# Kernel optimization log

Hardware: AMD Instinct MI355X
Metric: run time of the kernel (lower is better)

Reference implementation:

```python
import jax, jax.numpy as jnp
import numpy as np

B, S, D, FF, E, K = 32, 32, 768, 3072, 8, 2


def setup_inputs() -> dict:
    key = jax.random.key(0)
    ks = jax.random.split(key, 6)
    rn = lambda k, shape, sc: (jax.random.normal(k, shape, dtype=jnp.float32) * sc)
    return {
        "x": rn(ks[0], (B, S, D), 1.0),
        "attention_mask": jnp.ones((B, S), dtype=jnp.float32),
        "Wg": rn(ks[1], (D, E), 0.02),          # gate Linear weight
        "bg": jnp.zeros((E,), jnp.float32),      # gate Linear bias
        "W1": rn(ks[2], (E, D, FF), 0.02),       # per-expert FFN up-proj
        "b1": jnp.zeros((E, FF), jnp.float32),
        "W2": rn(ks[3], (E, FF, D), 0.02),       # per-expert FFN down-proj
        "b2": jnp.zeros((E, D), jnp.float32),
    }


def reference(x, attention_mask, Wg, bg, W1, b1, W2, b2):
    # --- sentence-level gating (source overwrites mask with ones) ---
    mask = jnp.ones_like(attention_mask)                      # [B,S]
    x_avg = (x * mask[..., None]).sum(1) / mask[..., None].sum(1)  # [B,D]
    logits_gate = x_avg @ Wg + bg                             # [B,E]
    prob_gate = jax.nn.softmax(logits_gate, axis=-1)
    select_prob_gate, gate = jax.lax.top_k(prob_gate, K)      # [B,K], [B,K]

    # --- per-expert FFN on all sentences (dense equivalent of the
    #     sort/split/vstack dispatch in the source) ---
    # h: [E,B,S,FF]
    h = jnp.einsum('bsd,edf->ebsf', x, W1) + b1[:, None, None, :]
    h = jax.nn.gelu(h, approximate=False)
    out = jnp.einsum('ebsf,efd->ebsd', h, W2) + b2[:, None, None, :]  # [E,B,S,D]

    # --- combine: the source sums the topk expert outputs UNWEIGHTED
    #     (tmp_prob is computed but never applied) ---
    sel = jax.nn.one_hot(gate, E, dtype=x.dtype).sum(1)       # [B,E], entries in {0,1}
    moe_result = jnp.einsum('be,ebsd->bsd', sel, out)         # [B,S,D]

    return moe_result, select_prob_gate, gate
```

## Files before the change

kernel.cpp:

```cpp
#include <hip/hip_runtime.h>
#include <hip/hip_bf16.h>
#include <math.h>

#define BB 32
#define SS 32
#define DD 768
#define FFD 3072
#define EE 8
#define KK 2
#define NPAIR 64
#define MAXT 22

typedef __attribute__((ext_vector_type(8))) short short8;
typedef __attribute__((ext_vector_type(4))) float f32x4;
typedef __attribute__((ext_vector_type(8))) unsigned short us8;


#define H_OFF    4096
#define XBF_OFF  (H_OFF + 12582912)
#define PART_OFF XBF_OFF
#define PZ       (2048 * 768)
#define WS_MAIN  ((size_t)PART_OFF + 4ull * PZ * 2ull)

__device__ __forceinline__ unsigned short f2bf(float f) {
    __hip_bfloat16 h = __float2bfloat16(f);
    return __builtin_bit_cast(unsigned short, h);
}
__device__ __forceinline__ float bf2f(unsigned short u) {
    __hip_bfloat16 h = __builtin_bit_cast(__hip_bfloat16, u);
    return __bfloat162float(h);
}

__device__ __forceinline__ int lds_off(int row, int byte_in_row) {
    return row * 128 + (byte_in_row ^ ((row & 7) << 4));
}

__device__ __forceinline__ void phase_barrier() {
    __builtin_amdgcn_sched_barrier(0);
    asm volatile("s_waitcnt lgkmcnt(0)" ::: "memory");
    __builtin_amdgcn_s_barrier();
    __builtin_amdgcn_sched_barrier(0);
}

__global__ __launch_bounds__(256) void gate_kernel(
    const float* __restrict__ x, const float* __restrict__ Wg,
    const float* __restrict__ bg, float* __restrict__ out,
    int* __restrict__ gates)
{
    int b = blockIdx.x;
    int tid = threadIdx.x;

    float acc[EE];
#pragma unroll
    for (int e = 0; e < EE; ++e) acc[e] = 0.f;

    for (int d = tid; d < DD; d += 256) {
        float xs = 0.f;
        const float* xp = x + (size_t)b * SS * DD + d;
#pragma unroll
        for (int s = 0; s < SS; ++s) xs += xp[(size_t)s * DD];
#pragma unroll
        for (int e = 0; e < EE; ++e) acc[e] += xs * Wg[d * EE + e];
    }

    __shared__ float red[EE][256];
#pragma unroll
    for (int e = 0; e < EE; ++e) red[e][tid] = acc[e];
    __syncthreads();
    for (int off = 128; off > 0; off >>= 1) {
        if (tid < off) {
#pragma unroll
            for (int e = 0; e < EE; ++e) red[e][tid] += red[e][tid + off];
        }
        __syncthreads();
    }

    if (tid == 0) {
        float lg[EE], p[EE];
        float m = -1e30f;
#pragma unroll
        for (int e = 0; e < EE; ++e) {
            lg[e] = red[e][0] / (float)SS + bg[e];
            m = fmaxf(m, lg[e]);
        }
        float sum = 0.f;
#pragma unroll
        for (int e = 0; e < EE; ++e) { p[e] = expf(lg[e] - m); sum += p[e]; }
        float inv = 1.f / sum;
#pragma unroll
        for (int e = 0; e < EE; ++e) p[e] *= inv;

        int i1 = 0;
        for (int e = 1; e < EE; ++e) if (p[e] > p[i1]) i1 = e;
        int i2 = (i1 == 0) ? 1 : 0;
        for (int e = 0; e < EE; ++e) if (e != i1 && p[e] > p[i2]) i2 = e;

        float* prob_out = out + (size_t)BB * SS * DD;
        float* gate_out = prob_out + BB * KK;
        prob_out[b * KK + 0] = p[i1];
        prob_out[b * KK + 1] = p[i2];
        gate_out[b * KK + 0] = (float)i1;
        gate_out[b * KK + 1] = (float)i2;
        gates[b * KK + 0] = i1;
        gates[b * KK + 1] = i2;
    }
}

__global__ __launch_bounds__(64) void sched_kernel(int* __restrict__ wsi)
{
    __shared__ int g[NPAIR];
    __shared__ int cnt[EE];
    __shared__ int start[EE + 1];
    int p = threadIdx.x;

    g[p] = wsi[p];
    __syncthreads();

    if (p < EE) {
        int c = 0;
        for (int q = 0; q < NPAIR; ++q) c += (g[q] == p);
        cnt[p] = c;
    }
    __syncthreads();
    if (p == 0) {
        start[0] = 0;
        for (int e = 0; e < EE; ++e) start[e + 1] = start[e] + cnt[e];
    }
    __syncthreads();

    int e = g[p];
    int rank = 0;
    for (int q = 0; q < NPAIR; ++q) rank += (q < p) && (g[q] == e);
    int slot = start[e] + rank;
    wsi[64 + slot] = p;
    wsi[200 + p] = slot;

    if (p == 0) {
        int t = 0;
        for (int e2 = 0; e2 < EE; ++e2) {
            for (int o = 0; o < cnt[e2]; o += 4) {
                wsi[128 + t] = e2;
                wsi[152 + t] = start[e2] + o;
                wsi[176 + t] = (cnt[e2] - o) < 4 ? (cnt[e2] - o) : 4;
                ++t;
            }
        }
        for (; t < MAXT; ++t) wsi[176 + t] = 0;
    }
}

__global__ __launch_bounds__(256) void pack_x(
    const float* __restrict__ x, unsigned short* __restrict__ xbf)
{
    int i = blockIdx.x * 256 + threadIdx.x;
    const float4* src = (const float4*)(x + (size_t)i * 8);
    float4 v0 = src[0], v1 = src[1];
    us8 u;
    u[0] = f2bf(v0.x); u[1] = f2bf(v0.y); u[2] = f2bf(v0.z); u[3] = f2bf(v0.w);
    u[4] = f2bf(v1.x); u[5] = f2bf(v1.y); u[6] = f2bf(v1.z); u[7] = f2bf(v1.w);
    *(us8*)(xbf + (size_t)i * 8) = u;
}

__global__ __launch_bounds__(256) void init_kernel(
    const int* __restrict__ gates, const float* __restrict__ b2,
    float* __restrict__ out)
{
    int idx = blockIdx.x * 256 + threadIdx.x;
    if (idx >= BB * SS * DD) return;
    int b = idx / (SS * DD);
    int d = idx % DD;
    int e0 = gates[b * KK + 0];
    int e1 = gates[b * KK + 1];
    out[idx] = b2[e0 * DD + d] + b2[e1 * DD + d];
}

__global__ __launch_bounds__(256, 2) void up_gemm(
    const unsigned short* __restrict__ xbf, const float* __restrict__ W1,
    const float* __restrict__ b1, const int* __restrict__ wsi,
    unsigned short* __restrict__ H)
{
    int bid = blockIdx.x;
    int xcd = bid & 7;
    int r = bid >> 3;
    int tile = r % MAXT;
    int grp = r / MAXT;
    int nt = grp * 8 + xcd;
    int np = wsi[176 + tile];
    if (np == 0) return;
    int e = wsi[128 + tile];
    int slot0 = wsi[152 + tile];
    int tid = threadIdx.x;
    int wid = tid >> 6, lane = tid & 63;
    int wm = wid >> 1, wn = wid & 1;

    __shared__ char lds[65536];

    const unsigned short* asrc[4];
    int aoff[4];
#pragma unroll
    for (int i = 0; i < 4; ++i) {
        int c = tid + i * 256;
        int row = c >> 3, ch = c & 7;
        int lp = row >> 5;
        int lpc = lp < np ? lp : np - 1;
        int pair = wsi[64 + slot0 + lpc];
        int b = pair >> 1;
        asrc[i] = xbf + ((size_t)(b * SS + (row & 31))) * DD + ch * 8;
        aoff[i] = lds_off(row, ch * 16);
    }
    int n = tid & 127, kq = tid >> 7;
    const float* bsrc = W1 + ((size_t)e * DD + kq * 32) * FFD + nt * 128 + n;
    int boff[4];
#pragma unroll
    for (int m4 = 0; m4 < 4; ++m4) boff[m4] = lds_off(n, kq * 64 + m4 * 16);

    f32x4 acc[4][4];
#pragma unroll
    for (int i = 0; i < 4; ++i)
#pragma unroll
        for (int j = 0; j < 4; ++j) acc[i][j] = (f32x4)0.f;

    float bB0[32], bB1[32];
    us8 bA0[4], bA1[4];

    auto issue = [&](int k0, float (&bB)[32], us8 (&bA)[4]) {
        const float* wp = bsrc + (size_t)k0 * FFD;
#pragma unroll
        for (int j = 0; j < 32; ++j) bB[j] = wp[(size_t)j * FFD];
#pragma unroll
        for (int i = 0; i < 4; ++i) bA[i] = *(const us8*)(asrc[i] + k0);
    };
    auto store = [&](int p, const float (&bB)[32], const us8 (&bA)[4]) {
        char* Al = lds + p * 32768;
        char* Bl = Al + 16384;
#pragma unroll
        for (int i = 0; i < 4; ++i) *(us8*)(Al + aoff[i]) = bA[i];
#pragma unroll
        for (int m4 = 0; m4 < 4; ++m4) {
            us8 u;
#pragma unroll
            for (int m = 0; m < 8; ++m) u[m] = f2bf(bB[m4 * 8 + m]);
            *(us8*)(Bl + boff[m4]) = u;
        }
    };
    auto compute = [&](int p) {
        char* Al = lds + p * 32768;
        char* Bl = Al + 16384;
#pragma unroll
        for (int kk = 0; kk < 2; ++kk) {
            int kb = kk * 64 + (lane >> 4) * 16;
            short8 af[4], bf[4];
#pragma unroll
            for (int mf = 0; mf < 4; ++mf)
                af[mf] = *(short8*)(Al + lds_off(wm * 64 + mf * 16 + (lane & 15), kb));
#pragma unroll
            for (int nf = 0; nf < 4; ++nf)
                bf[nf] = *(short8*)(Bl + lds_off(wn * 64 + nf * 16 + (lane & 15), kb));
#pragma unroll
            for (int mf = 0; mf < 4; ++mf)
#pragma unroll
                for (int nf = 0; nf < 4; ++nf)
                    acc[mf][nf] = __builtin_amdgcn_mfma_f32_16x16x32_bf16(
                        af[mf], bf[nf], acc[mf][nf], 0, 0, 0);
        }
    };

    const int steps = 12;
    issue(0, bB0, bA0);
    issue(64, bB1, bA1);
    store(0, bB0, bA0);
    phase_barrier();
    for (int s = 0; s < steps; s += 2) {
        compute(0);
        if (s + 2 < steps) issue((s + 2) * 64, bB0, bA0);
        store(1, bB1, bA1);
        phase_barrier();
        compute(1);
        if (s + 2 < steps) {
            if (s + 3 < steps) issue((s + 3) * 64, bB1, bA1);
            store(0, bB0, bA0);
        }
        phase_barrier();
    }

    float bias[4];
#pragma unroll
    for (int nf = 0; nf < 4; ++nf)
        bias[nf] = b1[e * FFD + nt * 128 + wn * 64 + nf * 16 + (lane & 15)];
#pragma unroll
    for (int mf = 0; mf < 4; ++mf) {
#pragma unroll
        for (int i = 0; i < 4; ++i) {
            int row = wm * 64 + mf * 16 + (lane >> 4) * 4 + i;
            if ((row >> 5) >= np) continue;
            size_t srow = (size_t)(slot0 * 32 + row);
#pragma unroll
            for (int nf = 0; nf < 4; ++nf) {
                int f = nt * 128 + wn * 64 + nf * 16 + (lane & 15);
                float h = acc[mf][nf][i] + bias[nf];
                float g = 0.5f * h * (1.0f + erff(h * 0.70710678118654752f));
                H[srow * FFD + f] = f2bf(g);
            }
        }
    }
}

template<int MODE>
__global__ __launch_bounds__(256, 2) void down_gemm(
    const unsigned short* __restrict__ H, const float* __restrict__ W2,
    const int* __restrict__ wsi, unsigned short* __restrict__ part,
    float* __restrict__ out)
{
    int bid = blockIdx.x;
    int xcd = bid & 7;
    int r = bid >> 3;
    int tile = r % MAXT;
    int grp = r / MAXT;
    int pairidx = grp * 8 + xcd;
    int nt = pairidx % 6;
    int z = pairidx / 6;
    int np = wsi[176 + tile];
    if (np == 0) return;
    int e = wsi[128 + tile];
    int slot0 = wsi[152 + tile];
    int zb = z * (FFD / 4);
    int tid = threadIdx.x;
    int wid = tid >> 6, lane = tid & 63;
    int wm = wid >> 1, wn = wid & 1;

    __shared__ char lds[65536];

    const unsigned short* asrc[4];
    int aoff[4];
#pragma unroll
    for (int i = 0; i < 4; ++i) {
        int c = tid + i * 256;
        int row = c >> 3, ch = c & 7;
        int rc = row < np * 32 ? row : np * 32 - 1;
        asrc[i] = H + (size_t)(slot0 * 32 + rc) * FFD + zb + ch * 8;
        aoff[i] = lds_off(row, ch * 16);
    }
    int n = tid & 127, kq = tid >> 7;
    const float* bsrc = W2 + ((size_t)e * FFD + zb + kq * 32) * DD + nt * 128 + n;
    int boff[4];
#pragma unroll
    for (int m4 = 0; m4 < 4; ++m4) boff[m4] = lds_off(n, kq * 64 + m4 * 16);

    f32x4 acc[4][4];
#pragma unroll
    for (int i = 0; i < 4; ++i)
#pragma unroll
        for (int j = 0; j < 4; ++j) acc[i][j] = (f32x4)0.f;

    float bB0[32], bB1[32];
    us8 bA0[4], bA1[4];

    auto issue = [&](int k0, float (&bB)[32], us8 (&bA)[4]) {
        const float* wp = bsrc + (size_t)k0 * DD;
#pragma unroll
        for (int j = 0; j < 32; ++j) bB[j] = wp[(size_t)j * DD];
#pragma unroll
        for (int i = 0; i < 4; ++i) bA[i] = *(const us8*)(asrc[i] + k0);
    };
    auto store = [&](int p, const float (&bB)[32], const us8 (&bA)[4]) {
        char* Al = lds + p * 32768;
        char* Bl = Al + 16384;
#pragma unroll
        for (int i = 0; i < 4; ++i) *(us8*)(Al + aoff[i]) = bA[i];
#pragma unroll
        for (int m4 = 0; m4 < 4; ++m4) {
            us8 u;
#pragma unroll
            for (int m = 0; m < 8; ++m) u[m] = f2bf(bB[m4 * 8 + m]);
            *(us8*)(Bl + boff[m4]) = u;
        }
    };
    auto compute = [&](int p) {
        char* Al = lds + p * 32768;
        char* Bl = Al + 16384;
#pragma unroll
        for (int kk = 0; kk < 2; ++kk) {
            int kb = kk * 64 + (lane >> 4) * 16;
            short8 af[4], bf[4];
#pragma unroll
            for (int mf = 0; mf < 4; ++mf)
                af[mf] = *(short8*)(Al + lds_off(wm * 64 + mf * 16 + (lane & 15), kb));
#pragma unroll
            for (int nf = 0; nf < 4; ++nf)
                bf[nf] = *(short8*)(Bl + lds_off(wn * 64 + nf * 16 + (lane & 15), kb));
#pragma unroll
            for (int mf = 0; mf < 4; ++mf)
#pragma unroll
                for (int nf = 0; nf < 4; ++nf)
                    acc[mf][nf] = __builtin_amdgcn_mfma_f32_16x16x32_bf16(
                        af[mf], bf[nf], acc[mf][nf], 0, 0, 0);
        }
    };

    const int steps = 12;
    issue(0, bB0, bA0);
    issue(64, bB1, bA1);
    store(0, bB0, bA0);
    __syncthreads();
    for (int s = 0; s < steps; s += 2) {
        compute(0);
        if (s + 2 < steps) issue((s + 2) * 64, bB0, bA0);
        store(1, bB1, bA1);
        __syncthreads();
        compute(1);
        if (s + 2 < steps) {
            if (s + 3 < steps) issue((s + 3) * 64, bB1, bA1);
            store(0, bB0, bA0);
        }
        __syncthreads();
    }

#pragma unroll
    for (int mf = 0; mf < 4; ++mf) {
#pragma unroll
        for (int i = 0; i < 4; ++i) {
            int row = wm * 64 + mf * 16 + (lane >> 4) * 4 + i;
            int lp = row >> 5;
            if (lp >= np) continue;
            int col = nt * 128 + wn * 64 + (lane & 15);
            if (MODE == 0) {
                size_t srow = (size_t)(slot0 * 32 + row);
                unsigned short* pp = part + (size_t)z * PZ + srow * DD + col;
#pragma unroll
                for (int nf = 0; nf < 4; ++nf) pp[nf * 16] = f2bf(acc[mf][nf][i]);
            } else {
                int pair = wsi[64 + slot0 + lp];
                int b = pair >> 1;
                int sI = row & 31;
                float* op = out + ((size_t)(b * SS + sI)) * DD + col;
#pragma unroll
                for (int nf = 0; nf < 4; ++nf)
                    atomicAdd(op + nf * 16, acc[mf][nf][i]);
            }
        }
    }
}

__global__ __launch_bounds__(512) void reduce_kernel(
    const unsigned short* __restrict__ part, const int* __restrict__ wsi,
    const float* __restrict__ b2, float* __restrict__ out)
{
    int i8 = blockIdx.x * 512 + threadIdx.x;
    int flat = i8 * 8;
    int b = flat / (SS * DD);
    int r = flat - b * (SS * DD);
    int s = r / DD;
    int d = r - s * DD;

    int e0 = wsi[b * KK + 0];
    int e1 = wsi[b * KK + 1];
    int sl0 = wsi[200 + b * KK + 0];
    int sl1 = wsi[200 + b * KK + 1];
    size_t r0 = (size_t)(sl0 * 32 + s) * DD + d;
    size_t r1 = (size_t)(sl1 * 32 + s) * DD + d;

    const float* bb0 = b2 + e0 * DD + d;
    const float* bb1 = b2 + e1 * DD + d;

    float v[8];
#pragma unroll
    for (int j = 0; j < 8; ++j) v[j] = bb0[j] + bb1[j];
#pragma unroll
    for (int z = 0; z < 4; ++z) {
        us8 p0 = *(const us8*)(part + (size_t)z * PZ + r0);
        us8 p1 = *(const us8*)(part + (size_t)z * PZ + r1);
#pragma unroll
        for (int j = 0; j < 8; ++j) v[j] += bf2f(p0[j]) + bf2f(p1[j]);
    }
    float4* op = (float4*)(out + flat);
    op[0] = make_float4(v[0], v[1], v[2], v[3]);
    op[1] = make_float4(v[4], v[5], v[6], v[7]);
}

extern "C" void kernel_launch(void* const* d_in, const int* in_sizes, int n_in,
                              void* d_out, int out_size, void* d_ws, size_t ws_size,
                              hipStream_t stream) {
    const float* x  = (const float*)d_in[0];
    const float* Wg = (const float*)d_in[2];
    const float* bg = (const float*)d_in[3];
    const float* W1 = (const float*)d_in[4];
    const float* b1 = (const float*)d_in[5];
    const float* W2 = (const float*)d_in[6];
    const float* b2 = (const float*)d_in[7];
    float* out = (float*)d_out;

    int* wsi = (int*)d_ws;
    unsigned short* H    = (unsigned short*)((char*)d_ws + H_OFF);
    unsigned short* xbf  = (unsigned short*)((char*)d_ws + XBF_OFF);
    unsigned short* part = (unsigned short*)((char*)d_ws + PART_OFF);

    gate_kernel<<<BB, 256, 0, stream>>>(x, Wg, bg, out, wsi);
    sched_kernel<<<1, 64, 0, stream>>>(wsi);
    pack_x<<<(BB * SS * DD) / (256 * 8), 256, 0, stream>>>(x, xbf);
    up_gemm<<<8 * MAXT * 3, 256, 0, stream>>>(xbf, W1, b1, wsi, H);

    if (ws_size >= WS_MAIN) {
        down_gemm<0><<<8 * MAXT * 3, 256, 0, stream>>>(H, W2, wsi, part, out);
        reduce_kernel<<<(BB * SS * DD) / (512 * 8), 512, 0, stream>>>(
            part, wsi, b2, out);
    } else {
        init_kernel<<<(BB * SS * DD + 255) / 256, 256, 0, stream>>>(wsi, b2, out);
        down_gemm<1><<<8 * MAXT * 3, 256, 0, stream>>>(H, W2, wsi, part, out);
    }
}
```

Measured before the change: 82.49 us.

## Use 512-thread blocks and load activation fragments directly from global memory

Both expert GEMMs move from 256 to 512 threads per block with 8 waves in a 2x4 layout, each wave covering a 64x32 sub-tile instead of 64x64. The bf16 activation (A) operand is no longer staged through LDS; each wave reads its MFMA fragments straight from global memory. LDS then holds only the double-buffered weight tile, halving shared memory per block and raising the occupancy target. The trade-off is more global/L2 traffic and latency exposure on the A loads, since fragments are re-read by each wave without prefetching. The custom phase barrier is replaced by __syncthreads.

```diff
diff --git a/kernel.cpp b/kernel.cpp
--- a/kernel.cpp
+++ b/kernel.cpp
@@ -33,13 +33,6 @@
 
 __device__ __forceinline__ int lds_off(int row, int byte_in_row) {
     return row * 128 + (byte_in_row ^ ((row & 7) << 4));
-}
-
-__device__ __forceinline__ void phase_barrier() {
-    __builtin_amdgcn_sched_barrier(0);
-    asm volatile("s_waitcnt lgkmcnt(0)" ::: "memory");
-    __builtin_amdgcn_s_barrier();
-    __builtin_amdgcn_sched_barrier(0);
 }
 
 __global__ __launch_bounds__(256) void gate_kernel(
@@ -174,7 +167,7 @@
     out[idx] = b2[e0 * DD + d] + b2[e1 * DD + d];
 }
 
-__global__ __launch_bounds__(256, 2) void up_gemm(
+__global__ __launch_bounds__(512, 4) void up_gemm(
     const unsigned short* __restrict__ xbf, const float* __restrict__ W1,
     const float* __restrict__ b1, const int* __restrict__ wsi,
     unsigned short* __restrict__ H)
@@ -191,102 +184,90 @@
     int slot0 = wsi[152 + tile];
     int tid = threadIdx.x;
     int wid = tid >> 6, lane = tid & 63;
-    int wm = wid >> 1, wn = wid & 1;
-
-    __shared__ char lds[65536];
-
-    const unsigned short* asrc[4];
-    int aoff[4];
-#pragma unroll
-    for (int i = 0; i < 4; ++i) {
-        int c = tid + i * 256;
-        int row = c >> 3, ch = c & 7;
+    int wm = wid >> 2, wn = wid & 3;
+
+    __shared__ char lds[32768];
+
+    const unsigned short* apL[4];
+#pragma unroll
+    for (int mf = 0; mf < 4; ++mf) {
+        int row = wm * 64 + mf * 16 + (lane & 15);
         int lp = row >> 5;
         int lpc = lp < np ? lp : np - 1;
         int pair = wsi[64 + slot0 + lpc];
-        int b = pair >> 1;
-        asrc[i] = xbf + ((size_t)(b * SS + (row & 31))) * DD + ch * 8;
-        aoff[i] = lds_off(row, ch * 16);
-    }
+        apL[mf] = xbf + ((size_t)((pair >> 1) * SS + (row & 31))) * DD
+                + (lane >> 4) * 8;
+    }
+
     int n = tid & 127, kq = tid >> 7;
-    const float* bsrc = W1 + ((size_t)e * DD + kq * 32) * FFD + nt * 128 + n;
-    int boff[4];
-#pragma unroll
-    for (int m4 = 0; m4 < 4; ++m4) boff[m4] = lds_off(n, kq * 64 + m4 * 16);
-
-    f32x4 acc[4][4];
+    const float* bsrc = W1 + ((size_t)e * DD + kq * 16) * FFD + nt * 128 + n;
+    int boff0 = lds_off(n, kq * 32);
+    int boff1 = lds_off(n, kq * 32 + 16);
+
+    f32x4 acc[4][2];
 #pragma unroll
     for (int i = 0; i < 4; ++i)
 #pragma unroll
-        for (int j = 0; j < 4; ++j) acc[i][j] = (f32x4)0.f;
-
-    float bB0[32], bB1[32];
-    us8 bA0[4], bA1[4];
-
-    auto issue = [&](int k0, float (&bB)[32], us8 (&bA)[4]) {
+        for (int j = 0; j < 2; ++j) acc[i][j] = (f32x4)0.f;
+
+    float bB0[16], bB1[16];
+
+    auto issue = [&](int k0, float (&bB)[16]) {
         const float* wp = bsrc + (size_t)k0 * FFD;
 #pragma unroll
-        for (int j = 0; j < 32; ++j) bB[j] = wp[(size_t)j * FFD];
-#pragma unroll
-        for (int i = 0; i < 4; ++i) bA[i] = *(const us8*)(asrc[i] + k0);
-    };
-    auto store = [&](int p, const float (&bB)[32], const us8 (&bA)[4]) {
-        char* Al = lds + p * 32768;
-        char* Bl = Al + 16384;
-#pragma unroll
-        for (int i = 0; i < 4; ++i) *(us8*)(Al + aoff[i]) = bA[i];
-#pragma unroll
-        for (int m4 = 0; m4 < 4; ++m4) {
-            us8 u;
-#pragma unroll
-            for (int m = 0; m < 8; ++m) u[m] = f2bf(bB[m4 * 8 + m]);
-            *(us8*)(Bl + boff[m4]) = u;
-        }
-    };
-    auto compute = [&](int p) {
-        char* Al = lds + p * 32768;
-        char* Bl = Al + 16384;
+        for (int j = 0; j < 16; ++j) bB[j] = wp[(size_t)j * FFD];
+    };
+    auto store = [&](int p, const float (&bB)[16]) {
+        char* Bl = lds + p * 16384;
+        us8 u0, u1;
+#pragma unroll
+        for (int m = 0; m < 8; ++m) { u0[m] = f2bf(bB[m]); u1[m] = f2bf(bB[8 + m]); }
+        *(us8*)(Bl + boff0) = u0;
+        *(us8*)(Bl + boff1) = u1;
+    };
+    auto compute = [&](int p, int k0) {
+        char* Bl = lds + p * 16384;
 #pragma unroll
         for (int kk = 0; kk < 2; ++kk) {
             int kb = kk * 64 + (lane >> 4) * 16;
-            short8 af[4], bf[4];
+            short8 af[4], bf[2];
 #pragma unroll
             for (int mf = 0; mf < 4; ++mf)
-                af[mf] = *(short8*)(Al + lds_off(wm * 64 + mf * 16 + (lane & 15), kb));
-#pragma unroll
-            for (int nf = 0; nf < 4; ++nf)
-                bf[nf] = *(short8*)(Bl + lds_off(wn * 64 + nf * 16 + (lane & 15), kb));
+                af[mf] = *(const short8*)(apL[mf] + k0 + kk * 32);
+#pragma unroll
+            for (int nf = 0; nf < 2; ++nf)
+                bf[nf] = *(short8*)(Bl + lds_off(wn * 32 + nf * 16 + (lane & 15), kb));
 #pragma unroll
             for (int mf = 0; mf < 4; ++mf)
 #pragma unroll
-                for (int nf = 0; nf < 4; ++nf)
+                for (int nf = 0; nf < 2; ++nf)
                     acc[mf][nf] = __builtin_amdgcn_mfma_f32_16x16x32_bf16(
                         af[mf], bf[nf], acc[mf][nf], 0, 0, 0);
         }
     };
 
     const int steps = 12;
-    issue(0, bB0, bA0);
-    issue(64, bB1, bA1);
-    store(0, bB0, bA0);
-    phase_barrier();
+    issue(0, bB0);
+    issue(64, bB1);
+    store(0, bB0);
+    __syncthreads();
     for (int s = 0; s < steps; s += 2) {
-        compute(0);
-        if (s + 2 < steps) issue((s + 2) * 64, bB0, bA0);
-        store(1, bB1, bA1);
-        phase_barrier();
-        compute(1);
+        compute(0, s * 64);
+        if (s + 2 < steps) issue((s + 2) * 64, bB0);
+        store(1, bB1);
+        __syncthreads();
+        compute(1, (s + 1) * 64);
         if (s + 2 < steps) {
-            if (s + 3 < steps) issue((s + 3) * 64, bB1, bA1);
-            store(0, bB0, bA0);
-        }
-        phase_barrier();
-    }
-
-    float bias[4];
-#pragma unroll
-    for (int nf = 0; nf < 4; ++nf)
-        bias[nf] = b1[e * FFD + nt * 128 + wn * 64 + nf * 16 + (lane & 15)];
+            if (s + 3 < steps) issue((s + 3) * 64, bB1);
+            store(0, bB0);
+        }
+        __syncthreads();
+    }
+
+    float bias[2];
+#pragma unroll
+    for (int nf = 0; nf < 2; ++nf)
+        bias[nf] = b1[e * FFD + nt * 128 + wn * 32 + nf * 16 + (lane & 15)];
 #pragma unroll
     for (int mf = 0; mf < 4; ++mf) {
 #pragma unroll
@@ -295,8 +276,8 @@
             if ((row >> 5) >= np) continue;
             size_t srow = (size_t)(slot0 * 32 + row);
 #pragma unroll
-            for (int nf = 0; nf < 4; ++nf) {
-                int f = nt * 128 + wn * 64 + nf * 16 + (lane & 15);
+            for (int nf = 0; nf < 2; ++nf) {
+                int f = nt * 128 + wn * 32 + nf * 16 + (lane & 15);
                 float h = acc[mf][nf][i] + bias[nf];
                 float g = 0.5f * h * (1.0f + erff(h * 0.70710678118654752f));
                 H[srow * FFD + f] = f2bf(g);
@@ -306,7 +287,7 @@
 }
 
 template<int MODE>
-__global__ __launch_bounds__(256, 2) void down_gemm(
+__global__ __launch_bounds__(512, 4) void down_gemm(
     const unsigned short* __restrict__ H, const float* __restrict__ W2,
     const int* __restrict__ wsi, unsigned short* __restrict__ part,
     float* __restrict__ out)
@@ -315,7 +296,8 @@
     int xcd = bid & 7;
     int r = bid >> 3;
     int tile = r % MAXT;
-    int grp = r / MAXT;
+    int grp = r >> 3 ? 0 : 0;
+    grp = (bid >> 3) / MAXT;
     int pairidx = grp * 8 + xcd;
     int nt = pairidx % 6;
     int z = pairidx / 6;
@@ -326,91 +308,79 @@
     int zb = z * (FFD / 4);
     int tid = threadIdx.x;
     int wid = tid >> 6, lane = tid & 63;
-    int wm = wid >> 1, wn = wid & 1;
-
-    __shared__ char lds[65536];
-
-    const unsigned short* asrc[4];
-    int aoff[4];
-#pragma unroll
-    for (int i = 0; i < 4; ++i) {
-        int c = tid + i * 256;
-        int row = c >> 3, ch = c & 7;
+    int wm = wid >> 2, wn = wid & 3;
+
+    __shared__ char lds[32768];
+
+    const unsigned short* apL[4];
+#pragma unroll
+    for (int mf = 0; mf < 4; ++mf) {
+        int row = wm * 64 + mf * 16 + (lane & 15);
         int rc = row < np * 32 ? row : np * 32 - 1;
-        asrc[i] = H + (size_t)(slot0 * 32 + rc) * FFD + zb + ch * 8;
-        aoff[i] = lds_off(row, ch * 16);
-    }
+        apL[mf] = H + (size_t)(slot0 * 32 + rc) * FFD + zb + (lane >> 4) * 8;
+    }
+
     int n = tid & 127, kq = tid >> 7;
-    const float* bsrc = W2 + ((size_t)e * FFD + zb + kq * 32) * DD + nt * 128 + n;
-    int boff[4];
-#pragma unroll
-    for (int m4 = 0; m4 < 4; ++m4) boff[m4] = lds_off(n, kq * 64 + m4 * 16);
-
-    f32x4 acc[4][4];
+    const float* bsrc = W2 + ((size_t)e * FFD + zb + kq * 16) * DD + nt * 128 + n;
+    int boff0 = lds_off(n, kq * 32);
+    int boff1 = lds_off(n, kq * 32 + 16);
+
+    f32x4 acc[4][2];
 #pragma unroll
     for (int i = 0; i < 4; ++i)
 #pragma unroll
-        for (int j = 0; j < 4; ++j) acc[i][j] = (f32x4)0.f;
-
-    float bB0[32], bB1[32];
-    us8 bA0[4], bA1[4];
-
-    auto issue = [&](int k0, float (&bB)[32], us8 (&bA)[4]) {
+        for (int j = 0; j < 2; ++j) acc[i][j] = (f32x4)0.f;
+
+    float bB0[16], bB1[16];
+
+    auto issue = [&](int k0, float (&bB)[16]) {
         const float* wp = bsrc + (size_t)k0 * DD;
 #pragma unroll
-        for (int j = 0; j < 32; ++j) bB[j] = wp[(size_t)j * DD];
-#pragma unroll
-        for (int i = 0; i < 4; ++i) bA[i] = *(const us8*)(asrc[i] + k0);
-    };
-    auto store = [&](int p, const float (&bB)[32], const us8 (&bA)[4]) {
-        char* Al = lds + p * 32768;
-        char* Bl = Al + 16384;
-#pragma unroll
-        for (int i = 0; i < 4; ++i) *(us8*)(Al + aoff[i]) = bA[i];
-#pragma unroll
-        for (int m4 = 0; m4 < 4; ++m4) {
-            us8 u;
-#pragma unroll
-            for (int m = 0; m < 8; ++m) u[m] = f2bf(bB[m4 * 8 + m]);
-            *(us8*)(Bl + boff[m4]) = u;
-        }
-    };
-    auto compute = [&](int p) {
-        char* Al = lds + p * 32768;
-        char* Bl = Al + 16384;
+        for (int j = 0; j < 16; ++j) bB[j] = wp[(size_t)j * DD];
+    };
+    auto store = [&](int p, const float (&bB)[16]) {
+        char* Bl = lds + p * 16384;
+        us8 u0, u1;
+#pragma unroll
+        for (int m = 0; m < 8; ++m) { u0[m] = f2bf(bB[m]); u1[m] = f2bf(bB[8 + m]); }
+        *(us8*)(Bl + boff0) = u0;
+        *(us8*)(Bl + boff1) = u1;
+    };
+    auto compute = [&](int p, int k0) {
+        char* Bl = lds + p * 16384;
 #pragma unroll
         for (int kk = 0; kk < 2; ++kk) {
             int kb = kk * 64 + (lane >> 4) * 16;
-            short8 af[4], bf[4];
+            short8 af[4], bf[2];
 #pragma unroll
             for (int mf = 0; mf < 4; ++mf)
-                af[mf] = *(short8*)(Al + lds_off(wm * 64 + mf * 16 + (lane & 15), kb));
-#pragma unroll
-            for (int nf = 0; nf < 4; ++nf)
-                bf[nf] = *(short8*)(Bl + lds_off(wn * 64 + nf * 16 + (lane & 15), kb));
+                af[mf] = *(const short8*)(apL[mf] + k0 + kk * 32);
+#pragma unroll
+            for (int nf = 0; nf < 2; ++nf)
+                bf[nf] = *(short8*)(Bl + lds_off(wn * 32 + nf * 16 + (lane & 15), kb));
 #pragma unroll
             for (int mf = 0; mf < 4; ++mf)
 #pragma unroll
-                for (int nf = 0; nf < 4; ++nf)
+                for (int nf = 0; nf < 2; ++nf)
                     acc[mf][nf] = __builtin_amdgcn_mfma_f32_16x16x32_bf16(
                         af[mf], bf[nf], acc[mf][nf], 0, 0, 0);
         }
     };
 
     const int steps = 12;
-    issue(0, bB0, bA0);
-    issue(64, bB1, bA1);
-    store(0, bB0, bA0);
+    issue(0, bB0);
+    issue(64, bB1);
+    store(0, bB0);
     __syncthreads();
     for (int s = 0; s < steps; s += 2) {
-        compute(0);
-        if (s + 2 < steps) issue((s + 2) * 64, bB0, bA0);
-        store(1, bB1, bA1);
+        compute(0, s * 64);
+        if (s + 2 < steps) issue((s + 2) * 64, bB0);
+        store(1, bB1);
         __syncthreads();
-        compute(1);
+        compute(1, (s + 1) * 64);
         if (s + 2 < steps) {
-            if (s + 3 < steps) issue((s + 3) * 64, bB1, bA1);
-            store(0, bB0, bA0);
+            if (s + 3 < steps) issue((s + 3) * 64, bB1);
+            store(0, bB0);
         }
         __syncthreads();
     }
@@ -422,19 +392,19 @@
             int row = wm * 64 + mf * 16 + (lane >> 4) * 4 + i;
             int lp = row >> 5;
             if (lp >= np) continue;
-            int col = nt * 128 + wn * 64 + (lane & 15);
+            int col = nt * 128 + wn * 32 + (lane & 15);
             if (MODE == 0) {
                 size_t srow = (size_t)(slot0 * 32 + row);
                 unsigned short* pp = part + (size_t)z * PZ + srow * DD + col;
 #pragma unroll
-                for (int nf = 0; nf < 4; ++nf) pp[nf * 16] = f2bf(acc[mf][nf][i]);
+                for (int nf = 0; nf < 2; ++nf) pp[nf * 16] = f2bf(acc[mf][nf][i]);
             } else {
                 int pair = wsi[64 + slot0 + lp];
                 int b = pair >> 1;
                 int sI = row & 31;
                 float* op = out + ((size_t)(b * SS + sI)) * DD + col;
 #pragma unroll
-                for (int nf = 0; nf < 4; ++nf)
+                for (int nf = 0; nf < 2; ++nf)
                     atomicAdd(op + nf * 16, acc[mf][nf][i]);
             }
         }
@@ -497,14 +467,14 @@
     gate_kernel<<<BB, 256, 0, stream>>>(x, Wg, bg, out, wsi);
     sched_kernel<<<1, 64, 0, stream>>>(wsi);
     pack_x<<<(BB * SS * DD) / (256 * 8), 256, 0, stream>>>(x, xbf);
-    up_gemm<<<8 * MAXT * 3, 256, 0, stream>>>(xbf, W1, b1, wsi, H);
+    up_gemm<<<8 * MAXT * 3, 512, 0, stream>>>(xbf, W1, b1, wsi, H);
 
     if (ws_size >= WS_MAIN) {
-        down_gemm<0><<<8 * MAXT * 3, 256, 0, stream>>>(H, W2, wsi, part, out);
+        down_gemm<0><<<8 * MAXT * 3, 512, 0, stream>>>(H, W2, wsi, part, out);
         reduce_kernel<<<(BB * SS * DD) / (512 * 8), 512, 0, stream>>>(
             part, wsi, b2, out);
     } else {
         init_kernel<<<(BB * SS * DD + 255) / 256, 256, 0, stream>>>(wsi, b2, out);
-        down_gemm<1><<<8 * MAXT * 3, 256, 0, stream>>>(H, W2, wsi, part, out);
-    }
-}
+        down_gemm<1><<<8 * MAXT * 3, 512, 0, stream>>>(H, W2, wsi, part, out);
+    }
+}
```

Measured after the change: 133.5 us. 61.8% more time.

## Halve up-projection M tile to two sentence pairs with a finer tile schedule

Applied to the files above, without the earlier changes.

The scheduler now also builds a second tile list that groups at most 2 (rather than 4) sentence-pairs per expert tile. up_gemm uses this list, shrinking each block's M tile from 128 to 64 rows, with all four waves splitting N instead of a 2x2 wave grid. LDS per block drops and launch bounds are raised to 3 blocks per CU, giving more blocks and less padding waste on partially filled tiles. The cost is that each W1 column tile is fetched and converted from fp32 by roughly twice as many blocks. The custom phase barrier is also replaced with __syncthreads.

```diff
diff --git a/kernel.cpp b/kernel.cpp
--- a/kernel.cpp
+++ b/kernel.cpp
@@ -10,6 +10,7 @@
 #define KK 2
 #define NPAIR 64
 #define MAXT 22
+#define MAXT2 36
 
 typedef __attribute__((ext_vector_type(8))) short short8;
 typedef __attribute__((ext_vector_type(4))) float f32x4;
@@ -33,13 +34,6 @@
 
 __device__ __forceinline__ int lds_off(int row, int byte_in_row) {
     return row * 128 + (byte_in_row ^ ((row & 7) << 4));
-}
-
-__device__ __forceinline__ void phase_barrier() {
-    __builtin_amdgcn_sched_barrier(0);
-    asm volatile("s_waitcnt lgkmcnt(0)" ::: "memory");
-    __builtin_amdgcn_s_barrier();
-    __builtin_amdgcn_sched_barrier(0);
 }
 
 __global__ __launch_bounds__(256) void gate_kernel(
@@ -147,6 +141,18 @@
         }
         for (; t < MAXT; ++t) wsi[176 + t] = 0;
     }
+    if (p == 1) {
+        int t = 0;
+        for (int e2 = 0; e2 < EE; ++e2) {
+            for (int o = 0; o < cnt[e2]; o += 2) {
+                wsi[300 + t] = e2;
+                wsi[340 + t] = start[e2] + o;
+                wsi[380 + t] = (cnt[e2] - o) < 2 ? (cnt[e2] - o) : 2;
+                ++t;
+            }
+        }
+        for (; t < MAXT2; ++t) wsi[380 + t] = 0;
+    }
 }
 
 __global__ __launch_bounds__(256) void pack_x(
@@ -174,7 +180,7 @@
     out[idx] = b2[e0 * DD + d] + b2[e1 * DD + d];
 }
 
-__global__ __launch_bounds__(256, 2) void up_gemm(
+__global__ __launch_bounds__(256, 3) void up_gemm(
     const unsigned short* __restrict__ xbf, const float* __restrict__ W1,
     const float* __restrict__ b1, const int* __restrict__ wsi,
     unsigned short* __restrict__ H)
@@ -182,23 +188,23 @@
     int bid = blockIdx.x;
     int xcd = bid & 7;
     int r = bid >> 3;
-    int tile = r % MAXT;
-    int grp = r / MAXT;
+    int tile = r % MAXT2;
+    int grp = r / MAXT2;
     int nt = grp * 8 + xcd;
-    int np = wsi[176 + tile];
+    int np = wsi[380 + tile];
     if (np == 0) return;
-    int e = wsi[128 + tile];
-    int slot0 = wsi[152 + tile];
+    int e = wsi[300 + tile];
+    int slot0 = wsi[340 + tile];
     int tid = threadIdx.x;
     int wid = tid >> 6, lane = tid & 63;
-    int wm = wid >> 1, wn = wid & 1;
-
-    __shared__ char lds[65536];
-
-    const unsigned short* asrc[4];
-    int aoff[4];
-#pragma unroll
-    for (int i = 0; i < 4; ++i) {
+    int wn = wid;
+
+    __shared__ char lds[49152];
+
+    const unsigned short* asrc[2];
+    int aoff[2];
+#pragma unroll
+    for (int i = 0; i < 2; ++i) {
         int c = tid + i * 256;
         int row = c >> 3, ch = c & 7;
         int lp = row >> 5;
@@ -214,27 +220,27 @@
 #pragma unroll
     for (int m4 = 0; m4 < 4; ++m4) boff[m4] = lds_off(n, kq * 64 + m4 * 16);
 
-    f32x4 acc[4][4];
+    f32x4 acc[4][2];
 #pragma unroll
     for (int i = 0; i < 4; ++i)
 #pragma unroll
-        for (int j = 0; j < 4; ++j) acc[i][j] = (f32x4)0.f;
+        for (int j = 0; j < 2; ++j) acc[i][j] = (f32x4)0.f;
 
     float bB0[32], bB1[32];
-    us8 bA0[4], bA1[4];
-
-    auto issue = [&](int k0, float (&bB)[32], us8 (&bA)[4]) {
+    us8 bA0[2], bA1[2];
+
+    auto issue = [&](int k0, float (&bB)[32], us8 (&bA)[2]) {
         const float* wp = bsrc + (size_t)k0 * FFD;
 #pragma unroll
         for (int j = 0; j < 32; ++j) bB[j] = wp[(size_t)j * FFD];
 #pragma unroll
-        for (int i = 0; i < 4; ++i) bA[i] = *(const us8*)(asrc[i] + k0);
+        for (int i = 0; i < 2; ++i) bA[i] = *(const us8*)(asrc[i] + k0);
     };
-    auto store = [&](int p, const float (&bB)[32], const us8 (&bA)[4]) {
-        char* Al = lds + p * 32768;
-        char* Bl = Al + 16384;
-#pragma unroll
-        for (int i = 0; i < 4; ++i) *(us8*)(Al + aoff[i]) = bA[i];
+    auto store = [&](int p, const float (&bB)[32], const us8 (&bA)[2]) {
+        char* Al = lds + p * 24576;
+        char* Bl = Al + 8192;
+#pragma unroll
+        for (int i = 0; i < 2; ++i) *(us8*)(Al + aoff[i]) = bA[i];
 #pragma unroll
         for (int m4 = 0; m4 < 4; ++m4) {
             us8 u;
@@ -244,22 +250,22 @@
         }
     };
     auto compute = [&](int p) {
-        char* Al = lds + p * 32768;
-        char* Bl = Al + 16384;
+        char* Al = lds + p * 24576;
+        char* Bl = Al + 8192;
 #pragma unroll
         for (int kk = 0; kk < 2; ++kk) {
             int kb = kk * 64 + (lane >> 4) * 16;
-            short8 af[4], bf[4];
+            short8 af[4], bf[2];
 #pragma unroll
             for (int mf = 0; mf < 4; ++mf)
-                af[mf] = *(short8*)(Al + lds_off(wm * 64 + mf * 16 + (lane & 15), kb));
-#pragma unroll
-            for (int nf = 0; nf < 4; ++nf)
-                bf[nf] = *(short8*)(Bl + lds_off(wn * 64 + nf * 16 + (lane & 15), kb));
+                af[mf] = *(short8*)(Al + lds_off(mf * 16 + (lane & 15), kb));
+#pragma unroll
+            for (int nf = 0; nf < 2; ++nf)
+                bf[nf] = *(short8*)(Bl + lds_off(wn * 32 + nf * 16 + (lane & 15), kb));
 #pragma unroll
             for (int mf = 0; mf < 4; ++mf)
 #pragma unroll
-                for (int nf = 0; nf < 4; ++nf)
+                for (int nf = 0; nf < 2; ++nf)
                     acc[mf][nf] = __builtin_amdgcn_mfma_f32_16x16x32_bf16(
                         af[mf], bf[nf], acc[mf][nf], 0, 0, 0);
         }
@@ -269,34 +275,34 @@
     issue(0, bB0, bA0);
     issue(64, bB1, bA1);
     store(0, bB0, bA0);
-    phase_barrier();
+    __syncthreads();
     for (int s = 0; s < steps; s += 2) {
         compute(0);
         if (s + 2 < steps) issue((s + 2) * 64, bB0, bA0);
         store(1, bB1, bA1);
-        phase_barrier();
+        __syncthreads();
         compute(1);
         if (s + 2 < steps) {
             if (s + 3 < steps) issue((s + 3) * 64, bB1, bA1);
             store(0, bB0, bA0);
         }
-        phase_barrier();
-    }
-
-    float bias[4];
-#pragma unroll
-    for (int nf = 0; nf < 4; ++nf)
-        bias[nf] = b1[e * FFD + nt * 128 + wn * 64 + nf * 16 + (lane & 15)];
+        __syncthreads();
+    }
+
+    float bias[2];
+#pragma unroll
+    for (int nf = 0; nf < 2; ++nf)
+        bias[nf] = b1[e * FFD + nt * 128 + wn * 32 + nf * 16 + (lane & 15)];
 #pragma unroll
     for (int mf = 0; mf < 4; ++mf) {
 #pragma unroll
         for (int i = 0; i < 4; ++i) {
-            int row = wm * 64 + mf * 16 + (lane >> 4) * 4 + i;
+            int row = mf * 16 + (lane >> 4) * 4 + i;
             if ((row >> 5) >= np) continue;
             size_t srow = (size_t)(slot0 * 32 + row);
 #pragma unroll
-            for (int nf = 0; nf < 4; ++nf) {
-                int f = nt * 128 + wn * 64 + nf * 16 + (lane & 15);
+            for (int nf = 0; nf < 2; ++nf) {
+                int f = nt * 128 + wn * 32 + nf * 16 + (lane & 15);
                 float h = acc[mf][nf][i] + bias[nf];
                 float g = 0.5f * h * (1.0f + erff(h * 0.70710678118654752f));
                 H[srow * FFD + f] = f2bf(g);
@@ -497,7 +503,7 @@
     gate_kernel<<<BB, 256, 0, stream>>>(x, Wg, bg, out, wsi);
     sched_kernel<<<1, 64, 0, stream>>>(wsi);
     pack_x<<<(BB * SS * DD) / (256 * 8), 256, 0, stream>>>(x, xbf);
-    up_gemm<<<8 * MAXT * 3, 256, 0, stream>>>(xbf, W1, b1, wsi, H);
+    up_gemm<<<8 * MAXT2 * 3, 256, 0, stream>>>(xbf, W1, b1, wsi, H);
 
     if (ws_size >= WS_MAIN) {
         down_gemm<0><<<8 * MAXT * 3, 256, 0, stream>>>(H, W2, wsi, part, out);
```

Result: slower. 93.29 us (+13.1%).

## Enlarge up-GEMM tiles to eight pairs with 512-thread blocks and K=32 steps

Applied to the files above, without the earlier changes.

The scheduler now also emits a second tile list grouping up to 8 sentence-expert pairs per tile (256 rows) instead of 4. The up-projection GEMM runs with 512 threads (8 waves in a 4x2 grid), so each fetched W1 column tile is reused across twice as many token rows, which is meant to halve redundant fp32 W1 reads. The K step shrinks from 64 to 32 so the double-buffered LDS fits, and the XOR swizzle is replaced by an 80-byte padded row stride. The cost is twice as many pipeline steps and barriers, and fewer, larger blocks that may be less balanced across CUs.

```diff
diff --git a/kernel.cpp b/kernel.cpp
--- a/kernel.cpp
+++ b/kernel.cpp
@@ -10,6 +10,7 @@
 #define KK 2
 #define NPAIR 64
 #define MAXT 22
+#define MAXT3 15
 
 typedef __attribute__((ext_vector_type(8))) short short8;
 typedef __attribute__((ext_vector_type(4))) float f32x4;
@@ -33,6 +34,9 @@
 
 __device__ __forceinline__ int lds_off(int row, int byte_in_row) {
     return row * 128 + (byte_in_row ^ ((row & 7) << 4));
+}
+__device__ __forceinline__ int off80(int row, int byte_in_row) {
+    return row * 80 + byte_in_row;
 }
 
 __device__ __forceinline__ void phase_barrier() {
@@ -147,6 +151,18 @@
         }
         for (; t < MAXT; ++t) wsi[176 + t] = 0;
     }
+    if (p == 1) {
+        int t = 0;
+        for (int e2 = 0; e2 < EE; ++e2) {
+            for (int o = 0; o < cnt[e2]; o += 8) {
+                wsi[270 + t] = e2;
+                wsi[290 + t] = start[e2] + o;
+                wsi[310 + t] = (cnt[e2] - o) < 8 ? (cnt[e2] - o) : 8;
+                ++t;
+            }
+        }
+        for (; t < MAXT3; ++t) wsi[310 + t] = 0;
+    }
 }
 
 __global__ __launch_bounds__(256) void pack_x(
@@ -174,7 +190,7 @@
     out[idx] = b2[e0 * DD + d] + b2[e1 * DD + d];
 }
 
-__global__ __launch_bounds__(256, 2) void up_gemm(
+__global__ __launch_bounds__(512, 2) void up_gemm(
     const unsigned short* __restrict__ xbf, const float* __restrict__ W1,
     const float* __restrict__ b1, const int* __restrict__ wsi,
     unsigned short* __restrict__ H)
@@ -182,37 +198,35 @@
     int bid = blockIdx.x;
     int xcd = bid & 7;
     int r = bid >> 3;
-    int tile = r % MAXT;
-    int grp = r / MAXT;
+    int tile = r % MAXT3;
+    int grp = r / MAXT3;
     int nt = grp * 8 + xcd;
-    int np = wsi[176 + tile];
+    int np = wsi[310 + tile];
     if (np == 0) return;
-    int e = wsi[128 + tile];
-    int slot0 = wsi[152 + tile];
+    int e = wsi[270 + tile];
+    int slot0 = wsi[290 + tile];
     int tid = threadIdx.x;
     int wid = tid >> 6, lane = tid & 63;
     int wm = wid >> 1, wn = wid & 1;
 
-    __shared__ char lds[65536];
-
-    const unsigned short* asrc[4];
-    int aoff[4];
-#pragma unroll
-    for (int i = 0; i < 4; ++i) {
-        int c = tid + i * 256;
-        int row = c >> 3, ch = c & 7;
+    __shared__ char lds[61440];
+
+    const unsigned short* asrc[2];
+    int aoff[2];
+#pragma unroll
+    for (int i = 0; i < 2; ++i) {
+        int c = tid + i * 512;
+        int row = c >> 2, ch = c & 3;
         int lp = row >> 5;
         int lpc = lp < np ? lp : np - 1;
         int pair = wsi[64 + slot0 + lpc];
         int b = pair >> 1;
         asrc[i] = xbf + ((size_t)(b * SS + (row & 31))) * DD + ch * 8;
-        aoff[i] = lds_off(row, ch * 16);
+        aoff[i] = off80(row, ch * 16);
     }
     int n = tid & 127, kq = tid >> 7;
-    const float* bsrc = W1 + ((size_t)e * DD + kq * 32) * FFD + nt * 128 + n;
-    int boff[4];
-#pragma unroll
-    for (int m4 = 0; m4 < 4; ++m4) boff[m4] = lds_off(n, kq * 64 + m4 * 16);
+    const float* bsrc = W1 + ((size_t)e * DD + kq * 8) * FFD + nt * 128 + n;
+    int boff = off80(n, kq * 16);
 
     f32x4 acc[4][4];
 #pragma unroll
@@ -220,64 +234,58 @@
 #pragma unroll
         for (int j = 0; j < 4; ++j) acc[i][j] = (f32x4)0.f;
 
-    float bB0[32], bB1[32];
-    us8 bA0[4], bA1[4];
-
-    auto issue = [&](int k0, float (&bB)[32], us8 (&bA)[4]) {
+    float bB0[8], bB1[8];
+    us8 bA0[2], bA1[2];
+
+    auto issue = [&](int k0, float (&bB)[8], us8 (&bA)[2]) {
         const float* wp = bsrc + (size_t)k0 * FFD;
 #pragma unroll
-        for (int j = 0; j < 32; ++j) bB[j] = wp[(size_t)j * FFD];
-#pragma unroll
-        for (int i = 0; i < 4; ++i) bA[i] = *(const us8*)(asrc[i] + k0);
+        for (int j = 0; j < 8; ++j) bB[j] = wp[(size_t)j * FFD];
+#pragma unroll
+        for (int i = 0; i < 2; ++i) bA[i] = *(const us8*)(asrc[i] + k0);
     };
-    auto store = [&](int p, const float (&bB)[32], const us8 (&bA)[4]) {
-        char* Al = lds + p * 32768;
-        char* Bl = Al + 16384;
-#pragma unroll
-        for (int i = 0; i < 4; ++i) *(us8*)(Al + aoff[i]) = bA[i];
-#pragma unroll
-        for (int m4 = 0; m4 < 4; ++m4) {
-            us8 u;
-#pragma unroll
-            for (int m = 0; m < 8; ++m) u[m] = f2bf(bB[m4 * 8 + m]);
-            *(us8*)(Bl + boff[m4]) = u;
-        }
+    auto store = [&](int p, const float (&bB)[8], const us8 (&bA)[2]) {
+        char* Al = lds + p * 30720;
+        char* Bl = Al + 20480;
+#pragma unroll
+        for (int i = 0; i < 2; ++i) *(us8*)(Al + aoff[i]) = bA[i];
+        us8 u;
+#pragma unroll
+        for (int m = 0; m < 8; ++m) u[m] = f2bf(bB[m]);
+        *(us8*)(Bl + boff) = u;
     };
     auto compute = [&](int p) {
-        char* Al = lds + p * 32768;
-        char* Bl = Al + 16384;
-#pragma unroll
-        for (int kk = 0; kk < 2; ++kk) {
-            int kb = kk * 64 + (lane >> 4) * 16;
-            short8 af[4], bf[4];
-#pragma unroll
-            for (int mf = 0; mf < 4; ++mf)
-                af[mf] = *(short8*)(Al + lds_off(wm * 64 + mf * 16 + (lane & 15), kb));
+        char* Al = lds + p * 30720;
+        char* Bl = Al + 20480;
+        int kb = (lane >> 4) * 16;
+        short8 af[4], bf[4];
+#pragma unroll
+        for (int mf = 0; mf < 4; ++mf)
+            af[mf] = *(short8*)(Al + off80(wm * 64 + mf * 16 + (lane & 15), kb));
+#pragma unroll
+        for (int nf = 0; nf < 4; ++nf)
+            bf[nf] = *(short8*)(Bl + off80(wn * 64 + nf * 16 + (lane & 15), kb));
+#pragma unroll
+        for (int mf = 0; mf < 4; ++mf)
 #pragma unroll
             for (int nf = 0; nf < 4; ++nf)
-                bf[nf] = *(short8*)(Bl + lds_off(wn * 64 + nf * 16 + (lane & 15), kb));
-#pragma unroll
-            for (int mf = 0; mf < 4; ++mf)
-#pragma unroll
-                for (int nf = 0; nf < 4; ++nf)
-                    acc[mf][nf] = __builtin_amdgcn_mfma_f32_16x16x32_bf16(
-                        af[mf], bf[nf], acc[mf][nf], 0, 0, 0);
-        }
+                acc[mf][nf] = __builtin_amdgcn_mfma_f32_16x16x32_bf16(
+                    af[mf], bf[nf], acc[mf][nf], 0, 0, 0);
     };
 
-    const int steps = 12;
+    const int steps = 24;
     issue(0, bB0, bA0);
-    issue(64, bB1, bA1);
+    issue(32, bB1, bA1);
     store(0, bB0, bA0);
     phase_barrier();
     for (int s = 0; s < steps; s += 2) {
         compute(0);
-        if (s + 2 < steps) issue((s + 2) * 64, bB0, bA0);
+        if (s + 2 < steps) issue((s + 2) * 32, bB0, bA0);
         store(1, bB1, bA1);
         phase_barrier();
         compute(1);
         if (s + 2 < steps) {
-            if (s + 3 < steps) issue((s + 3) * 64, bB1, bA1);
+            if (s + 3 < steps) issue((s + 3) * 32, bB1, bA1);
             store(0, bB0, bA0);
         }
         phase_barrier();
@@ -497,7 +505,7 @@
     gate_kernel<<<BB, 256, 0, stream>>>(x, Wg, bg, out, wsi);
     sched_kernel<<<1, 64, 0, stream>>>(wsi);
     pack_x<<<(BB * SS * DD) / (256 * 8), 256, 0, stream>>>(x, xbf);
-    up_gemm<<<8 * MAXT * 3, 256, 0, stream>>>(xbf, W1, b1, wsi, H);
+    up_gemm<<<8 * MAXT3 * 3, 512, 0, stream>>>(xbf, W1, b1, wsi, H);
 
     if (ws_size >= WS_MAIN) {
         down_gemm<0><<<8 * MAXT * 3, 256, 0, stream>>>(H, W2, wsi, part, out);
```

After: 102.7 us. +24.5%, slower.
